# Performance work log

Hardware: AMD Instinct MI355X
Metric: run time of the kernel (lower is better)

The kernel has to match this reference:

```python
import jax, jax.numpy as jnp
import numpy as np

B, L, D = 4, 2048, 1024   # batch, seq_len, input_channels
S = 4096                  # param_token_num
DV = 1024                 # output_channels


def setup_inputs() -> dict:
    key = jax.random.key(0)
    k1, k2, k3 = jax.random.split(key, 3)
    return {
        "inputs": jax.random.normal(k1, (B, L, D), dtype=jnp.float32),
        "key_param_tokens": jax.random.normal(k2, (S, D), dtype=jnp.float32),
        "value_param_tokens": jax.random.normal(k3, (S, DV), dtype=jnp.float32),
    }


def reference(inputs, key_param_tokens, value_param_tokens):
    # scores: [B, L, S] — full score matrix (this is what a fused kernel would avoid)
    scores = jnp.einsum("bld,sd->bls", inputs, key_param_tokens)
    # gelu_l2_norm: exact (erf) gelu, then L2-normalize over S and rescale by sqrt(S)
    g = jax.nn.gelu(scores, approximate=False)
    l2 = jnp.linalg.norm(g, axis=-1, keepdims=True)
    w = g / l2 * jnp.sqrt(jnp.asarray(g.shape[-1], g.dtype))
    # weighted sum over param value tokens: [B, L, DV]
    return jnp.einsum("bls,sv->blv", w, value_param_tokens)
```

## Files before the change

kernel.cpp:

```cpp
#include <hip/hip_runtime.h>
#include <hip/hip_bf16.h>
#include <stdint.h>

#define M_ROWS 8192
#define D_DIM  1024
#define S_DIM  4096
#define DV_DIM 1024

typedef __attribute__((ext_vector_type(8))) short bf16x8;
typedef __attribute__((ext_vector_type(4))) float f32x4;
typedef unsigned short u16;

static __device__ __forceinline__ u16 f2bf(float x) {
  union { float f; unsigned u; } v; v.f = x;
  unsigned r = v.u + 0x7FFFu + ((v.u >> 16) & 1u);
  return (u16)(r >> 16);
}
static __device__ __forceinline__ float bf2f(u16 h) {
  union { unsigned u; float f; } v; v.u = ((unsigned)h) << 16;
  return v.f;
}
static __device__ __forceinline__ float gelu_fast(float x) {
  float u = 0.7978845608028654f * x * (1.0f + 0.044715f * x * x);
  float e = __expf(2.0f * u);
  float t = 1.0f - 2.0f / (e + 1.0f);
  return 0.5f * x * (1.0f + t);
}

static __device__ __forceinline__ void gload16(const void* g, void* l) {
  __builtin_amdgcn_global_load_lds(
      (__attribute__((address_space(1))) void*)(void*)(g),
      (__attribute__((address_space(3))) void*)(l), 16, 0, 0);
}

__global__ __launch_bounds__(256)
void cast_f32_bf16(const float* __restrict__ in, u16* __restrict__ out, int n4) {
  const int i = blockIdx.x * 256 + threadIdx.x;
  if (i >= n4) return;
  const float4 v = ((const float4*)in)[i];
  ushort4 o;
  o.x = f2bf(v.x); o.y = f2bf(v.y); o.z = f2bf(v.z); o.w = f2bf(v.w);
  ((ushort4*)out)[i] = o;
}

__global__ __launch_bounds__(256)
void transpose_cast(const float* __restrict__ V, u16* __restrict__ VT, int R, int C) {
  __shared__ float tile[32][33];
  const int tx = threadIdx.x & 31;
  const int ty = threadIdx.x >> 5;
  const int r0 = blockIdx.y * 32;
  const int c0 = blockIdx.x * 32;
#pragma unroll
  for (int dy = 0; dy < 32; dy += 8)
    tile[ty + dy][tx] = V[(long)(r0 + ty + dy) * C + (c0 + tx)];
  __syncthreads();
#pragma unroll
  for (int dy = 0; dy < 32; dy += 8)
    VT[(long)(c0 + ty + dy) * R + (r0 + tx)] = f2bf(tile[tx][ty + dy]);
}

__global__ __launch_bounds__(256)
void row_scale(const u16* __restrict__ G, float* __restrict__ scale, int S) {
  const int row = blockIdx.x;
  const u16* g = G + (long)row * S;
  float ssq = 0.f;
  for (int i = threadIdx.x * 8; i < S; i += 256 * 8) {
    bf16x8 v = *(const bf16x8*)&g[i];
#pragma unroll
    for (int j = 0; j < 8; ++j) {
      float f = bf2f((u16)v[j]);
      ssq += f * f;
    }
  }
#pragma unroll
  for (int off = 32; off > 0; off >>= 1)
    ssq += __shfl_down(ssq, off, 64);
  __shared__ float wsum[4];
  if ((threadIdx.x & 63) == 0) wsum[threadIdx.x >> 6] = ssq;
  __syncthreads();
  if (threadIdx.x == 0) {
    float t = wsum[0] + wsum[1] + wsum[2] + wsum[3];
    scale[row] = 64.0f * rsqrtf(t + 1e-30f);
  }
}


#define VM4 asm volatile("s_waitcnt vmcnt(4)" ::: "memory")
#define VM2 asm volatile("s_waitcnt vmcnt(2)" ::: "memory")
#define VM0 asm volatile("s_waitcnt vmcnt(0)" ::: "memory")

#define PHASE(P, STAGES, WAITS)                                               \
  {                                                                           \
    bf16x8 af[2][2];                                                          \
    _Pragma("unroll")                                                         \
    for (int j = 0; j < 2; ++j) {                                             \
      const int ar = wm * 128 + ((P) * 2 + j) * 16 + fr;                      \
      af[j][0] = rdfrag(la, ar, 0);                                           \
      af[j][1] = rdfrag(la, ar, 1);                                           \
    }                                                                         \
    STAGES;                                                                   \
    __builtin_amdgcn_s_barrier();                                             \
    asm volatile("s_waitcnt lgkmcnt(0)" ::: "memory");                        \
    __builtin_amdgcn_sched_barrier(0);                                        \
    __builtin_amdgcn_s_setprio(1);                                            \
    _Pragma("unroll")                                                         \
    for (int j = 0; j < 2; ++j) {                                             \
      _Pragma("unroll")                                                       \
      for (int n = 0; n < NF; ++n) {                                          \
        acc[(P) * 2 + j][n] = __builtin_amdgcn_mfma_f32_16x16x32_bf16(        \
            af[j][0], bfr[n][0], acc[(P) * 2 + j][n], 0, 0, 0);               \
        acc[(P) * 2 + j][n] = __builtin_amdgcn_mfma_f32_16x16x32_bf16(        \
            af[j][1], bfr[n][1], acc[(P) * 2 + j][n], 0, 0, 0);               \
      }                                                                       \
    }                                                                         \
    __builtin_amdgcn_s_setprio(0);                                            \
    WAITS;                                                                    \
    __builtin_amdgcn_s_barrier();                                             \
  }

#define READ_B                                                                \
  {                                                                           \
    _Pragma("unroll")                                                         \
    for (int n = 0; n < NF; ++n) {                                            \
      const int br = wn * WNT + n * 16 + fr;                                  \
      bfr[n][0] = rdfrag(lb, br, 0);                                          \
      bfr[n][1] = rdfrag(lb, br, 1);                                          \
    }                                                                         \
  }

template <int MODE, int BN>
__global__ __launch_bounds__(512, 2)
void gemm8p(const u16* __restrict__ A, const u16* __restrict__ Bm,
            void* __restrict__ Cout, const float* __restrict__ scale,
            const int K, const int N, const int nBN, const int nWG) {
  constexpr int BM = 256, BK = 64;
  constexpr int WNT = BN / 4;
  constexpr int NF = WNT / 16;

  __shared__ u16 ldsA[2][BM * BK];
  __shared__ u16 ldsB[2][BN * BK];

  const int tid = threadIdx.x;
  const int lane = tid & 63;
  const int wv = tid >> 6;
  const int wm = wv >> 2, wn = wv & 3;
  const int fr = lane & 15, hi = lane >> 4;

  int wg;
  {
    const int q = nWG >> 3, r = nWG & 7;
    const int x = blockIdx.x & 7, ix = blockIdx.x >> 3;
    wg = (x < r ? x * (q + 1) : r * (q + 1) + (x - r) * q) + ix;
  }
  const int bm = wg / nBN, bn = wg % nBN;
  const long aR0 = (long)bm * BM;
  const long bR0 = (long)bn * BN;

  const int srow = tid >> 3;
  const int sch = (tid & 7) ^ (srow & 7);
  const long aoff = (aR0 + srow) * (long)K + sch * 8;
  const long boff = (bR0 + srow) * (long)K + sch * 8;

  auto SA = [&](int buf, int r, int kOff) {
    gload16(A + aoff + ((long)r * 64) * K + kOff, &ldsA[buf][r * 4096 + tid * 8]);
  };
  auto SB = [&](int buf, int r, int kOff) {
    gload16(Bm + boff + ((long)r * 64) * K + kOff, &ldsB[buf][r * 4096 + tid * 8]);
  };
  auto rdfrag = [&](const u16* base, int row, int kk) -> bf16x8 {
    return *(const bf16x8*)&base[row * 64 + (((kk << 2) | hi) ^ (row & 7)) * 8];
  };

  f32x4 acc[8][NF];
#pragma unroll
  for (int m = 0; m < 8; ++m)
#pragma unroll
    for (int n = 0; n < NF; ++n)
      acc[m][n] = f32x4{0.f, 0.f, 0.f, 0.f};

  bf16x8 bfr[NF][2];
  const int nK = K / BK;

  if constexpr (BN == 256) {
    SB(0, 0, 0); SB(0, 1, 0); SB(0, 2, 0); SB(0, 3, 0);
  } else {
    SB(0, 0, 0); SB(0, 1, 0);
  }
  SA(0, 0, 0); SA(0, 2, 0); SA(0, 1, 0); SA(0, 3, 0);
  VM2;
  __builtin_amdgcn_s_barrier();

  int cur = 0;
  for (int kt = 0; kt < nK - 1; ++kt) {
    const int kN = (kt + 1) * BK;
    const int nxt = cur ^ 1;
    const u16* la = ldsA[cur];
    const u16* lb = ldsB[cur];
    READ_B;
    if constexpr (BN == 256) {
      PHASE(0, { SB(nxt, 0, kN); SB(nxt, 1, kN); }, {});
      PHASE(1, { SB(nxt, 2, kN); SB(nxt, 3, kN); }, VM4);
      PHASE(2, { SA(nxt, 0, kN); SA(nxt, 2, kN); }, {});
      PHASE(3, { SA(nxt, 1, kN); SA(nxt, 3, kN); }, VM2);
    } else {
      PHASE(0, { SB(nxt, 0, kN); SB(nxt, 1, kN); }, {});
      PHASE(1, { SA(nxt, 0, kN); SA(nxt, 2, kN); }, VM4);
      PHASE(2, { SA(nxt, 1, kN); SA(nxt, 3, kN); }, {});
      PHASE(3, {}, VM2);
    }
    cur ^= 1;
  }

  {
    const u16* la = ldsA[cur];
    const u16* lb = ldsB[cur];
    READ_B;
    PHASE(0, {}, {});
    PHASE(1, {}, VM0);
    PHASE(2, {}, {});
    PHASE(3, {}, {});
  }

  const long row0 = aR0 + wm * 128;
  const long col0 = bR0 + wn * WNT;
  if constexpr (MODE == 0) {
    u16* Cg = (u16*)Cout;
#pragma unroll
    for (int m = 0; m < 8; ++m) {
#pragma unroll
      for (int i = 0; i < 4; ++i) {
        const long r = row0 + m * 16 + hi * 4 + i;
#pragma unroll
        for (int n = 0; n < NF; ++n)
          Cg[r * N + col0 + n * 16 + fr] = f2bf(gelu_fast(acc[m][n][i]));
      }
    }
  } else {
    float* Cf = (float*)Cout;
#pragma unroll
    for (int m = 0; m < 8; ++m) {
#pragma unroll
      for (int i = 0; i < 4; ++i) {
        const long r = row0 + m * 16 + hi * 4 + i;
        const float s = scale[r];
#pragma unroll
        for (int n = 0; n < NF; ++n)
          Cf[r * N + col0 + n * 16 + fr] = acc[m][n][i] * s;
      }
    }
  }
}

extern "C" void kernel_launch(void* const* d_in, const int* in_sizes, int n_in,
                              void* d_out, int out_size, void* d_ws, size_t ws_size,
                              hipStream_t stream) {
  const float* Qf = (const float*)d_in[0];
  const float* Kf = (const float*)d_in[1];
  const float* Vf = (const float*)d_in[2];
  float* Out = (float*)d_out;

  const int M = M_ROWS, D = D_DIM, S = S_DIM, DV = DV_DIM;

  char* p = (char*)d_ws;
  u16* Qb = (u16*)p;            p += (size_t)M * D * 2;
  u16* Kb = (u16*)p;            p += (size_t)S * D * 2;
  u16* VT = (u16*)p;            p += (size_t)DV * S * 2;
  float* scalebuf = (float*)p;  p += (size_t)M * 4;
  u16* G = (u16*)p;
  const size_t fixed = (size_t)(p - (char*)d_ws);
  const size_t avail = (ws_size > fixed) ? (ws_size - fixed) : 0;

  const size_t bytes_per_row = (size_t)S * 2;
  size_t rows_fit = avail / bytes_per_row;
  int chunk = (int)((rows_fit / 256) * 256);
  if (chunk > M) chunk = M;
  if (chunk < 256) chunk = 256;

  cast_f32_bf16<<<(M * D / 4 + 255) / 256, 256, 0, stream>>>(Qf, Qb, M * D / 4);
  cast_f32_bf16<<<(S * D / 4 + 255) / 256, 256, 0, stream>>>(Kf, Kb, S * D / 4);
  transpose_cast<<<dim3(DV / 32, S / 32), 256, 0, stream>>>(Vf, VT, S, DV);

  const int nBN1 = S / 256;
  const int nBN2 = DV / 128;
  for (int m0 = 0; m0 < M; m0 += chunk) {
    const int rows = (M - m0 < chunk) ? (M - m0) : chunk;
    const int nWG1 = (rows / 256) * nBN1;
    gemm8p<0, 256><<<dim3(nWG1), 512, 0, stream>>>(
        Qb + (size_t)m0 * D, Kb, (void*)G, nullptr, D, S, nBN1, nWG1);
    row_scale<<<rows, 256, 0, stream>>>(G, scalebuf, S);
    const int nWG2 = (rows / 256) * nBN2;
    gemm8p<1, 128><<<dim3(nWG2), 512, 0, stream>>>(
        G, VT, (void*)(Out + (size_t)m0 * DV), scalebuf, S, DV, nBN2, nWG2);
  }
}
```

Baseline: 197.5 us.

## Fuse row sum-of-squares into first GEMM epilogue and restructure prefetch pipeline

The first GEMM epilogue now accumulates the squared GELU values per row and tile, reduces them across lanes and waves through LDS, and writes per-tile partial sums. A small finalize kernel then turns these into row scales. This replaces the row_scale pass that re-read the full bf16 score matrix. The first GEMM also switches to a 2x4 wave layout instead of 4x2, and the K loop prefetches B two tiles ahead and A one tile ahead with retuned vmcnt waits. The risks are a larger epilogue, an extra partial-sum buffer, and subtle wait-count correctness in the new pipeline.

```diff
diff --git a/kernel.cpp b/kernel.cpp
--- a/kernel.cpp
+++ b/kernel.cpp
@@ -60,61 +60,44 @@
 }
 
 __global__ __launch_bounds__(256)
-void row_scale(const u16* __restrict__ G, float* __restrict__ scale, int S) {
-  const int row = blockIdx.x;
-  const u16* g = G + (long)row * S;
-  float ssq = 0.f;
-  for (int i = threadIdx.x * 8; i < S; i += 256 * 8) {
-    bf16x8 v = *(const bf16x8*)&g[i];
-#pragma unroll
-    for (int j = 0; j < 8; ++j) {
-      float f = bf2f((u16)v[j]);
-      ssq += f * f;
-    }
-  }
-#pragma unroll
-  for (int off = 32; off > 0; off >>= 1)
-    ssq += __shfl_down(ssq, off, 64);
-  __shared__ float wsum[4];
-  if ((threadIdx.x & 63) == 0) wsum[threadIdx.x >> 6] = ssq;
-  __syncthreads();
-  if (threadIdx.x == 0) {
-    float t = wsum[0] + wsum[1] + wsum[2] + wsum[3];
-    scale[row] = 64.0f * rsqrtf(t + 1e-30f);
-  }
-}
-
-
-#define VM4 asm volatile("s_waitcnt vmcnt(4)" ::: "memory")
-#define VM2 asm volatile("s_waitcnt vmcnt(2)" ::: "memory")
-#define VM0 asm volatile("s_waitcnt vmcnt(0)" ::: "memory")
-
-#define PHASE(P, STAGES, WAITS)                                               \
+void finalize_scale(const float* __restrict__ Pp, float* __restrict__ scale,
+                    int nBN, int rows) {
+  const int r = blockIdx.x * 256 + threadIdx.x;
+  if (r >= rows) return;
+  float s = 0.f;
+  for (int j = 0; j < nBN; ++j) s += Pp[(long)r * nBN + j];
+  scale[r] = 64.0f * rsqrtf(s + 1e-30f);
+}
+
+
+#define VMW(N) asm volatile("s_waitcnt vmcnt(" #N ")" ::: "memory")
+
+#define PH(P, STG, WT)                                                        \
   {                                                                           \
-    bf16x8 af[2][2];                                                          \
+    bf16x8 af[MF][2];                                                         \
     _Pragma("unroll")                                                         \
-    for (int j = 0; j < 2; ++j) {                                             \
-      const int ar = wm * 128 + ((P) * 2 + j) * 16 + fr;                      \
+    for (int j = 0; j < MF; ++j) {                                            \
+      const int ar = wm * MSPAN + ((P) * MF + j) * 16 + fr;                   \
       af[j][0] = rdfrag(la, ar, 0);                                           \
       af[j][1] = rdfrag(la, ar, 1);                                           \
     }                                                                         \
-    STAGES;                                                                   \
+    STG;                                                                      \
     __builtin_amdgcn_s_barrier();                                             \
     asm volatile("s_waitcnt lgkmcnt(0)" ::: "memory");                        \
     __builtin_amdgcn_sched_barrier(0);                                        \
     __builtin_amdgcn_s_setprio(1);                                            \
     _Pragma("unroll")                                                         \
-    for (int j = 0; j < 2; ++j) {                                             \
+    for (int j = 0; j < MF; ++j) {                                            \
       _Pragma("unroll")                                                       \
       for (int n = 0; n < NF; ++n) {                                          \
-        acc[(P) * 2 + j][n] = __builtin_amdgcn_mfma_f32_16x16x32_bf16(        \
-            af[j][0], bfr[n][0], acc[(P) * 2 + j][n], 0, 0, 0);               \
-        acc[(P) * 2 + j][n] = __builtin_amdgcn_mfma_f32_16x16x32_bf16(        \
-            af[j][1], bfr[n][1], acc[(P) * 2 + j][n], 0, 0, 0);               \
+        acc[(P) * MF + j][n] = __builtin_amdgcn_mfma_f32_16x16x32_bf16(       \
+            af[j][0], bfr[n][0], acc[(P) * MF + j][n], 0, 0, 0);              \
+        acc[(P) * MF + j][n] = __builtin_amdgcn_mfma_f32_16x16x32_bf16(       \
+            af[j][1], bfr[n][1], acc[(P) * MF + j][n], 0, 0, 0);              \
       }                                                                       \
     }                                                                         \
     __builtin_amdgcn_s_setprio(0);                                            \
-    WAITS;                                                                    \
+    WT;                                                                       \
     __builtin_amdgcn_s_barrier();                                             \
   }
 
@@ -122,20 +105,46 @@
   {                                                                           \
     _Pragma("unroll")                                                         \
     for (int n = 0; n < NF; ++n) {                                            \
-      const int br = wn * WNT + n * 16 + fr;                                  \
+      const int br = wn * NSPAN + n * 16 + fr;                                \
       bfr[n][0] = rdfrag(lb, br, 0);                                          \
       bfr[n][1] = rdfrag(lb, br, 1);                                          \
     }                                                                         \
   }
 
-template <int MODE, int BN>
+#define TILE(SAEN, SBEN, W1, W3)                                              \
+  {                                                                           \
+    const u16* la = ldsA[kt & 1];                                             \
+    const u16* lb = ldsB[kt & 1];                                             \
+    const int bA = (kt + 1) & 1;                                              \
+    const int bB = kt & 1;                                                    \
+    const long kA = (long)(kt + 1) * BK;                                      \
+    const long kB = (long)(kt + 2) * BK;                                      \
+    READ_B;                                                                   \
+    if constexpr (BN == 256) {                                                \
+      PH(0, if (SAEN) { SA(bA, 0, kA); SA(bA, 2, kA); }, {});                 \
+      PH(1, if (SAEN) { SA(bA, 1, kA); SA(bA, 3, kA); }, W1);                 \
+      PH(2, if (SBEN) { SB(bB, 0, kB); SB(bB, 1, kB); }, {});                 \
+      PH(3, if (SBEN) { SB(bB, 2, kB); SB(bB, 3, kB); }, W3);                 \
+    } else {                                                                  \
+      PH(0, if (SAEN) { SA(bA, 0, kA); SA(bA, 1, kA); }, {});                 \
+      PH(1, if (SAEN) { SA(bA, 2, kA); SA(bA, 3, kA); }, {});                 \
+      PH(2, if (SBEN) { SB(bB, 0, kB); SB(bB, 1, kB); }, {});                 \
+      PH(3, {}, W3);                                                          \
+    }                                                                         \
+  }
+
+template <int MODE, int BN, int WM>
 __global__ __launch_bounds__(512, 2)
 void gemm8p(const u16* __restrict__ A, const u16* __restrict__ Bm,
-            void* __restrict__ Cout, const float* __restrict__ scale,
+            void* __restrict__ Cout, float* __restrict__ Pp,
+            const float* __restrict__ scale,
             const int K, const int N, const int nBN, const int nWG) {
   constexpr int BM = 256, BK = 64;
-  constexpr int WNT = BN / 4;
-  constexpr int NF = WNT / 16;
+  constexpr int WN = 8 / WM;
+  constexpr int MSPAN = BM / WM;
+  constexpr int NSPAN = BN / WN;
+  constexpr int MF = MSPAN / 64;
+  constexpr int NF = NSPAN / 16;
 
   __shared__ u16 ldsA[2][BM * BK];
   __shared__ u16 ldsB[2][BN * BK];
@@ -143,7 +152,7 @@
   const int tid = threadIdx.x;
   const int lane = tid & 63;
   const int wv = tid >> 6;
-  const int wm = wv >> 2, wn = wv & 3;
+  const int wm = wv / WN, wn = wv % WN;
   const int fr = lane & 15, hi = lane >> 4;
 
   int wg;
@@ -161,19 +170,19 @@
   const long aoff = (aR0 + srow) * (long)K + sch * 8;
   const long boff = (bR0 + srow) * (long)K + sch * 8;
 
-  auto SA = [&](int buf, int r, int kOff) {
-    gload16(A + aoff + ((long)r * 64) * K + kOff, &ldsA[buf][r * 4096 + tid * 8]);
+  auto SA = [&](int buf, int r, long kOff) {
+    gload16(A + aoff + (long)r * 64 * K + kOff, &ldsA[buf][r * 4096 + tid * 8]);
   };
-  auto SB = [&](int buf, int r, int kOff) {
-    gload16(Bm + boff + ((long)r * 64) * K + kOff, &ldsB[buf][r * 4096 + tid * 8]);
+  auto SB = [&](int buf, int r, long kOff) {
+    gload16(Bm + boff + (long)r * 64 * K + kOff, &ldsB[buf][r * 4096 + tid * 8]);
   };
   auto rdfrag = [&](const u16* base, int row, int kk) -> bf16x8 {
     return *(const bf16x8*)&base[row * 64 + (((kk << 2) | hi) ^ (row & 7)) * 8];
   };
 
-  f32x4 acc[8][NF];
-#pragma unroll
-  for (int m = 0; m < 8; ++m)
+  f32x4 acc[4 * MF][NF];
+#pragma unroll
+  for (int m = 0; m < 4 * MF; ++m)
 #pragma unroll
     for (int n = 0; n < NF; ++n)
       acc[m][n] = f32x4{0.f, 0.f, 0.f, 0.f};
@@ -183,69 +192,67 @@
 
   if constexpr (BN == 256) {
     SB(0, 0, 0); SB(0, 1, 0); SB(0, 2, 0); SB(0, 3, 0);
+    SA(0, 0, 0); SA(0, 2, 0); SA(0, 1, 0); SA(0, 3, 0);
+    SB(1, 0, BK); SB(1, 1, BK); SB(1, 2, BK); SB(1, 3, BK);
+    VMW(6);
   } else {
     SB(0, 0, 0); SB(0, 1, 0);
-  }
-  SA(0, 0, 0); SA(0, 2, 0); SA(0, 1, 0); SA(0, 3, 0);
-  VM2;
+    SA(0, 0, 0); SA(0, 1, 0); SA(0, 2, 0); SA(0, 3, 0);
+    SB(1, 0, BK); SB(1, 1, BK);
+    VMW(2);
+  }
   __builtin_amdgcn_s_barrier();
 
-  int cur = 0;
-  for (int kt = 0; kt < nK - 1; ++kt) {
-    const int kN = (kt + 1) * BK;
-    const int nxt = cur ^ 1;
-    const u16* la = ldsA[cur];
-    const u16* lb = ldsB[cur];
-    READ_B;
-    if constexpr (BN == 256) {
-      PHASE(0, { SB(nxt, 0, kN); SB(nxt, 1, kN); }, {});
-      PHASE(1, { SB(nxt, 2, kN); SB(nxt, 3, kN); }, VM4);
-      PHASE(2, { SA(nxt, 0, kN); SA(nxt, 2, kN); }, {});
-      PHASE(3, { SA(nxt, 1, kN); SA(nxt, 3, kN); }, VM2);
-    } else {
-      PHASE(0, { SB(nxt, 0, kN); SB(nxt, 1, kN); }, {});
-      PHASE(1, { SA(nxt, 0, kN); SA(nxt, 2, kN); }, VM4);
-      PHASE(2, { SA(nxt, 1, kN); SA(nxt, 3, kN); }, {});
-      PHASE(3, {}, VM2);
-    }
-    cur ^= 1;
-  }
-
-  {
-    const u16* la = ldsA[cur];
-    const u16* lb = ldsB[cur];
-    READ_B;
-    PHASE(0, {}, {});
-    PHASE(1, {}, VM0);
-    PHASE(2, {}, {});
-    PHASE(3, {}, {});
-  }
-
-  const long row0 = aR0 + wm * 128;
-  const long col0 = bR0 + wn * WNT;
+  int kt = 0;
+  if constexpr (BN == 256) {
+    for (; kt < nK - 2; ++kt) TILE(true, true, VMW(8), VMW(6));
+    TILE(true, false, VMW(8), VMW(2)); ++kt;
+    TILE(false, false, VMW(0), {});
+  } else {
+    for (; kt < nK - 2; ++kt) TILE(true, true, {}, VMW(2));
+    TILE(true, false, {}, VMW(0)); ++kt;
+    TILE(false, false, {}, {});
+  }
+
   if constexpr (MODE == 0) {
     u16* Cg = (u16*)Cout;
-#pragma unroll
-    for (int m = 0; m < 8; ++m) {
+    float* red = (float*)&ldsA[0][0];
+#pragma unroll
+    for (int m = 0; m < 4 * MF; ++m) {
 #pragma unroll
       for (int i = 0; i < 4; ++i) {
-        const long r = row0 + m * 16 + hi * 4 + i;
-#pragma unroll
-        for (int n = 0; n < NF; ++n)
-          Cg[r * N + col0 + n * 16 + fr] = f2bf(gelu_fast(acc[m][n][i]));
+        const int rl = wm * MSPAN + m * 16 + hi * 4 + i;
+        const long r = aR0 + rl;
+        float s = 0.f;
+#pragma unroll
+        for (int n = 0; n < NF; ++n) {
+          const float g = gelu_fast(acc[m][n][i]);
+          Cg[r * N + bR0 + wn * NSPAN + n * 16 + fr] = f2bf(g);
+          s += g * g;
+        }
+        s += __shfl_xor(s, 1); s += __shfl_xor(s, 2);
+        s += __shfl_xor(s, 4); s += __shfl_xor(s, 8);
+        if (fr == 0) red[rl * WN + wn] = s;
       }
+    }
+    __syncthreads();
+    if (tid < BM) {
+      float s = 0.f;
+#pragma unroll
+      for (int w = 0; w < WN; ++w) s += red[tid * WN + w];
+      Pp[(aR0 + tid) * nBN + bn] = s;
     }
   } else {
     float* Cf = (float*)Cout;
 #pragma unroll
-    for (int m = 0; m < 8; ++m) {
+    for (int m = 0; m < 4 * MF; ++m) {
 #pragma unroll
       for (int i = 0; i < 4; ++i) {
-        const long r = row0 + m * 16 + hi * 4 + i;
+        const long r = aR0 + wm * MSPAN + m * 16 + hi * 4 + i;
         const float s = scale[r];
 #pragma unroll
         for (int n = 0; n < NF; ++n)
-          Cf[r * N + col0 + n * 16 + fr] = acc[m][n][i] * s;
+          Cf[r * N + bR0 + wn * NSPAN + n * 16 + fr] = acc[m][n][i] * s;
       }
     }
   }
@@ -260,12 +267,15 @@
   float* Out = (float*)d_out;
 
   const int M = M_ROWS, D = D_DIM, S = S_DIM, DV = DV_DIM;
+  const int nBN1 = S / 256;
+  const int nBN2 = DV / 128;
 
   char* p = (char*)d_ws;
   u16* Qb = (u16*)p;            p += (size_t)M * D * 2;
   u16* Kb = (u16*)p;            p += (size_t)S * D * 2;
   u16* VT = (u16*)p;            p += (size_t)DV * S * 2;
   float* scalebuf = (float*)p;  p += (size_t)M * 4;
+  float* Pp = (float*)p;        p += (size_t)M * nBN1 * 4;
   u16* G = (u16*)p;
   const size_t fixed = (size_t)(p - (char*)d_ws);
   const size_t avail = (ws_size > fixed) ? (ws_size - fixed) : 0;
@@ -280,16 +290,14 @@
   cast_f32_bf16<<<(S * D / 4 + 255) / 256, 256, 0, stream>>>(Kf, Kb, S * D / 4);
   transpose_cast<<<dim3(DV / 32, S / 32), 256, 0, stream>>>(Vf, VT, S, DV);
 
-  const int nBN1 = S / 256;
-  const int nBN2 = DV / 128;
   for (int m0 = 0; m0 < M; m0 += chunk) {
     const int rows = (M - m0 < chunk) ? (M - m0) : chunk;
     const int nWG1 = (rows / 256) * nBN1;
-    gemm8p<0, 256><<<dim3(nWG1), 512, 0, stream>>>(
-        Qb + (size_t)m0 * D, Kb, (void*)G, nullptr, D, S, nBN1, nWG1);
-    row_scale<<<rows, 256, 0, stream>>>(G, scalebuf, S);
+    gemm8p<0, 256, 2><<<dim3(nWG1), 512, 0, stream>>>(
+        Qb + (size_t)m0 * D, Kb, (void*)G, Pp, nullptr, D, S, nBN1, nWG1);
+    finalize_scale<<<(rows + 255) / 256, 256, 0, stream>>>(Pp, scalebuf, nBN1, rows);
     const int nWG2 = (rows / 256) * nBN2;
-    gemm8p<1, 128><<<dim3(nWG2), 512, 0, stream>>>(
-        G, VT, (void*)(Out + (size_t)m0 * DV), scalebuf, S, DV, nBN2, nWG2);
-  }
-}
+    gemm8p<1, 128, 4><<<dim3(nWG2), 512, 0, stream>>>(
+        G, VT, (void*)(Out + (size_t)m0 * DV), nullptr, scalebuf, S, DV, nBN2, nWG2);
+  }
+}
```

After: 215.9 us. 9.3% more time.

## Split-K second GEMM into two halves with 256-wide tiles plus reduction kernel

Applied to the files above, without the earlier changes.

The second GEMM (scaled G times V) is now split along K into two halves. Each half runs on separate workgroups with 256x256 tiles instead of 256x128, and the halves write to Out and a scratch buffer P1. An elementwise add kernel then sums the two partials. This keeps the same number of workgroups while using larger tiles for better operand reuse, at the cost of an extra fp32 partial write and read plus one more launch. The split path is taken only when the whole problem fits in one chunk and the workspace can hold the extra partial buffer.

```diff
diff --git a/kernel.cpp b/kernel.cpp
--- a/kernel.cpp
+++ b/kernel.cpp
@@ -81,6 +81,16 @@
   if (threadIdx.x == 0) {
     float t = wsum[0] + wsum[1] + wsum[2] + wsum[3];
     scale[row] = 64.0f * rsqrtf(t + 1e-30f);
+  }
+}
+
+__global__ __launch_bounds__(256)
+void add_inplace(float* __restrict__ Out, const float* __restrict__ P1, int n4) {
+  for (int i = blockIdx.x * 256 + threadIdx.x; i < n4; i += 2048 * 256) {
+    float4 a = ((const float4*)Out)[i];
+    const float4 b = ((const float4*)P1)[i];
+    a.x += b.x; a.y += b.y; a.z += b.z; a.w += b.w;
+    ((float4*)Out)[i] = a;
   }
 }
 
@@ -128,11 +138,13 @@
     }                                                                         \
   }
 
-template <int MODE, int BN>
+template <int MODE, int BN, bool SPLITK>
 __global__ __launch_bounds__(512, 2)
 void gemm8p(const u16* __restrict__ A, const u16* __restrict__ Bm,
-            void* __restrict__ Cout, const float* __restrict__ scale,
-            const int K, const int N, const int nBN, const int nWG) {
+            void* __restrict__ Cout0, void* __restrict__ Cout1,
+            const float* __restrict__ scale,
+            const int K, const int lda, const int ldb,
+            const int N, const int nBN, const int nWG) {
   constexpr int BM = 256, BK = 64;
   constexpr int WNT = BN / 4;
   constexpr int NF = WNT / 16;
@@ -152,20 +164,29 @@
     const int x = blockIdx.x & 7, ix = blockIdx.x >> 3;
     wg = (x < r ? x * (q + 1) : r * (q + 1) + (x - r) * q) + ix;
   }
+  void* Cout = Cout0;
+  if constexpr (SPLITK) {
+    const int half = nWG >> 1;
+    const int ks = (wg >= half) ? 1 : 0;
+    wg -= ks * half;
+    A += (long)ks * K;
+    Bm += (long)ks * K;
+    if (ks) Cout = Cout1;
+  }
   const int bm = wg / nBN, bn = wg % nBN;
   const long aR0 = (long)bm * BM;
   const long bR0 = (long)bn * BN;
 
   const int srow = tid >> 3;
   const int sch = (tid & 7) ^ (srow & 7);
-  const long aoff = (aR0 + srow) * (long)K + sch * 8;
-  const long boff = (bR0 + srow) * (long)K + sch * 8;
+  const long aoff = (aR0 + srow) * (long)lda + sch * 8;
+  const long boff = (bR0 + srow) * (long)ldb + sch * 8;
 
   auto SA = [&](int buf, int r, int kOff) {
-    gload16(A + aoff + ((long)r * 64) * K + kOff, &ldsA[buf][r * 4096 + tid * 8]);
+    gload16(A + aoff + ((long)r * 64) * lda + kOff, &ldsA[buf][r * 4096 + tid * 8]);
   };
   auto SB = [&](int buf, int r, int kOff) {
-    gload16(Bm + boff + ((long)r * 64) * K + kOff, &ldsB[buf][r * 4096 + tid * 8]);
+    gload16(Bm + boff + ((long)r * 64) * ldb + kOff, &ldsB[buf][r * 4096 + tid * 8]);
   };
   auto rdfrag = [&](const u16* base, int row, int kk) -> bf16x8 {
     return *(const bf16x8*)&base[row * 64 + (((kk << 2) | hi) ^ (row & 7)) * 8];
@@ -276,6 +297,11 @@
   if (chunk > M) chunk = M;
   if (chunk < 256) chunk = 256;
 
+  const size_t Gbytes = (size_t)M * S * 2;
+  const size_t Pbytes = (size_t)M * DV * 4;
+  const bool use_split = (chunk >= M) && (avail >= Gbytes + Pbytes);
+  float* P1 = (float*)((char*)G + Gbytes);
+
   cast_f32_bf16<<<(M * D / 4 + 255) / 256, 256, 0, stream>>>(Qf, Qb, M * D / 4);
   cast_f32_bf16<<<(S * D / 4 + 255) / 256, 256, 0, stream>>>(Kf, Kb, S * D / 4);
   transpose_cast<<<dim3(DV / 32, S / 32), 256, 0, stream>>>(Vf, VT, S, DV);
@@ -285,11 +311,19 @@
   for (int m0 = 0; m0 < M; m0 += chunk) {
     const int rows = (M - m0 < chunk) ? (M - m0) : chunk;
     const int nWG1 = (rows / 256) * nBN1;
-    gemm8p<0, 256><<<dim3(nWG1), 512, 0, stream>>>(
-        Qb + (size_t)m0 * D, Kb, (void*)G, nullptr, D, S, nBN1, nWG1);
+    gemm8p<0, 256, false><<<dim3(nWG1), 512, 0, stream>>>(
+        Qb + (size_t)m0 * D, Kb, (void*)G, nullptr, nullptr, D, D, D, S, nBN1, nWG1);
     row_scale<<<rows, 256, 0, stream>>>(G, scalebuf, S);
-    const int nWG2 = (rows / 256) * nBN2;
-    gemm8p<1, 128><<<dim3(nWG2), 512, 0, stream>>>(
-        G, VT, (void*)(Out + (size_t)m0 * DV), scalebuf, S, DV, nBN2, nWG2);
-  }
-}
+    if (use_split) {
+      const int nBNs = DV / 256;
+      const int nWGs = 2 * (M / 256) * nBNs;
+      gemm8p<1, 256, true><<<dim3(nWGs), 512, 0, stream>>>(
+          G, VT, (void*)Out, (void*)P1, scalebuf, S / 2, S, S, DV, nBNs, nWGs);
+      add_inplace<<<2048, 256, 0, stream>>>(Out, P1, M * DV / 4);
+    } else {
+      const int nWG2 = (rows / 256) * nBN2;
+      gemm8p<1, 128, false><<<dim3(nWG2), 512, 0, stream>>>(
+          G, VT, (void*)(Out + (size_t)m0 * DV), nullptr, scalebuf, S, S, S, DV, nBN2, nWG2);
+    }
+  }
+}
```

Result: faster. 192.5 us (-2.6%).

## Replace 256x256 8-wave GEMM tiles with 128x128 4-wave tiles

Applied to the files above, without the earlier changes.

Both GEMMs now use a single kernel with 128x128 output tiles and 256 threads (4 waves, each covering a 64x64 subtile) in place of the 8-wave 256-wide tiles. Each block loads half as many rows per stage, and the launch grid grows fourfold for the first GEMM and twofold for the second. The intent is to raise occupancy and block count for better load balance across CUs. The cost is lower arithmetic intensity per tile, so more global and LDS traffic per flop.

```diff
diff --git a/kernel.cpp b/kernel.cpp
--- a/kernel.cpp
+++ b/kernel.cpp
@@ -91,27 +91,20 @@
 
 #define PHASE(P, STAGES, WAITS)                                               \
   {                                                                           \
-    bf16x8 af[2][2];                                                          \
-    _Pragma("unroll")                                                         \
-    for (int j = 0; j < 2; ++j) {                                             \
-      const int ar = wm * 128 + ((P) * 2 + j) * 16 + fr;                      \
-      af[j][0] = rdfrag(la, ar, 0);                                           \
-      af[j][1] = rdfrag(la, ar, 1);                                           \
-    }                                                                         \
+    const int ar = wm * 64 + (P) * 16 + fr;                                   \
+    bf16x8 af0 = rdfrag(la, ar, 0);                                           \
+    bf16x8 af1 = rdfrag(la, ar, 1);                                           \
     STAGES;                                                                   \
     __builtin_amdgcn_s_barrier();                                             \
     asm volatile("s_waitcnt lgkmcnt(0)" ::: "memory");                        \
     __builtin_amdgcn_sched_barrier(0);                                        \
     __builtin_amdgcn_s_setprio(1);                                            \
     _Pragma("unroll")                                                         \
-    for (int j = 0; j < 2; ++j) {                                             \
-      _Pragma("unroll")                                                       \
-      for (int n = 0; n < NF; ++n) {                                          \
-        acc[(P) * 2 + j][n] = __builtin_amdgcn_mfma_f32_16x16x32_bf16(        \
-            af[j][0], bfr[n][0], acc[(P) * 2 + j][n], 0, 0, 0);               \
-        acc[(P) * 2 + j][n] = __builtin_amdgcn_mfma_f32_16x16x32_bf16(        \
-            af[j][1], bfr[n][1], acc[(P) * 2 + j][n], 0, 0, 0);               \
-      }                                                                       \
+    for (int n = 0; n < 4; ++n) {                                             \
+      acc[(P)][n] = __builtin_amdgcn_mfma_f32_16x16x32_bf16(                  \
+          af0, bfr[n][0], acc[(P)][n], 0, 0, 0);                              \
+      acc[(P)][n] = __builtin_amdgcn_mfma_f32_16x16x32_bf16(                  \
+          af1, bfr[n][1], acc[(P)][n], 0, 0, 0);                              \
     }                                                                         \
     __builtin_amdgcn_s_setprio(0);                                            \
     WAITS;                                                                    \
@@ -121,21 +114,19 @@
 #define READ_B                                                                \
   {                                                                           \
     _Pragma("unroll")                                                         \
-    for (int n = 0; n < NF; ++n) {                                            \
-      const int br = wn * WNT + n * 16 + fr;                                  \
+    for (int n = 0; n < 4; ++n) {                                             \
+      const int br = wn * 64 + n * 16 + fr;                                   \
       bfr[n][0] = rdfrag(lb, br, 0);                                          \
       bfr[n][1] = rdfrag(lb, br, 1);                                          \
     }                                                                         \
   }
 
-template <int MODE, int BN>
-__global__ __launch_bounds__(512, 2)
-void gemm8p(const u16* __restrict__ A, const u16* __restrict__ Bm,
+template <int MODE>
+__global__ __launch_bounds__(256, 2)
+void gemm4w(const u16* __restrict__ A, const u16* __restrict__ Bm,
             void* __restrict__ Cout, const float* __restrict__ scale,
             const int K, const int N, const int nBN, const int nWG) {
-  constexpr int BM = 256, BK = 64;
-  constexpr int WNT = BN / 4;
-  constexpr int NF = WNT / 16;
+  constexpr int BM = 128, BN = 128, BK = 64;
 
   __shared__ u16 ldsA[2][BM * BK];
   __shared__ u16 ldsB[2][BN * BK];
@@ -143,7 +134,7 @@
   const int tid = threadIdx.x;
   const int lane = tid & 63;
   const int wv = tid >> 6;
-  const int wm = wv >> 2, wn = wv & 3;
+  const int wm = wv >> 1, wn = wv & 1;
   const int fr = lane & 15, hi = lane >> 4;
 
   int wg;
@@ -162,30 +153,26 @@
   const long boff = (bR0 + srow) * (long)K + sch * 8;
 
   auto SA = [&](int buf, int r, int kOff) {
-    gload16(A + aoff + ((long)r * 64) * K + kOff, &ldsA[buf][r * 4096 + tid * 8]);
+    gload16(A + aoff + ((long)r * 32) * K + kOff, &ldsA[buf][r * 2048 + tid * 8]);
   };
   auto SB = [&](int buf, int r, int kOff) {
-    gload16(Bm + boff + ((long)r * 64) * K + kOff, &ldsB[buf][r * 4096 + tid * 8]);
+    gload16(Bm + boff + ((long)r * 32) * K + kOff, &ldsB[buf][r * 2048 + tid * 8]);
   };
   auto rdfrag = [&](const u16* base, int row, int kk) -> bf16x8 {
     return *(const bf16x8*)&base[row * 64 + (((kk << 2) | hi) ^ (row & 7)) * 8];
   };
 
-  f32x4 acc[8][NF];
-#pragma unroll
-  for (int m = 0; m < 8; ++m)
-#pragma unroll
-    for (int n = 0; n < NF; ++n)
+  f32x4 acc[4][4];
+#pragma unroll
+  for (int m = 0; m < 4; ++m)
+#pragma unroll
+    for (int n = 0; n < 4; ++n)
       acc[m][n] = f32x4{0.f, 0.f, 0.f, 0.f};
 
-  bf16x8 bfr[NF][2];
+  bf16x8 bfr[4][2];
   const int nK = K / BK;
 
-  if constexpr (BN == 256) {
-    SB(0, 0, 0); SB(0, 1, 0); SB(0, 2, 0); SB(0, 3, 0);
-  } else {
-    SB(0, 0, 0); SB(0, 1, 0);
-  }
+  SB(0, 0, 0); SB(0, 1, 0); SB(0, 2, 0); SB(0, 3, 0);
   SA(0, 0, 0); SA(0, 2, 0); SA(0, 1, 0); SA(0, 3, 0);
   VM2;
   __builtin_amdgcn_s_barrier();
@@ -197,17 +184,10 @@
     const u16* la = ldsA[cur];
     const u16* lb = ldsB[cur];
     READ_B;
-    if constexpr (BN == 256) {
-      PHASE(0, { SB(nxt, 0, kN); SB(nxt, 1, kN); }, {});
-      PHASE(1, { SB(nxt, 2, kN); SB(nxt, 3, kN); }, VM4);
-      PHASE(2, { SA(nxt, 0, kN); SA(nxt, 2, kN); }, {});
-      PHASE(3, { SA(nxt, 1, kN); SA(nxt, 3, kN); }, VM2);
-    } else {
-      PHASE(0, { SB(nxt, 0, kN); SB(nxt, 1, kN); }, {});
-      PHASE(1, { SA(nxt, 0, kN); SA(nxt, 2, kN); }, VM4);
-      PHASE(2, { SA(nxt, 1, kN); SA(nxt, 3, kN); }, {});
-      PHASE(3, {}, VM2);
-    }
+    PHASE(0, { SB(nxt, 0, kN); SB(nxt, 1, kN); }, {});
+    PHASE(1, { SB(nxt, 2, kN); SB(nxt, 3, kN); }, VM4);
+    PHASE(2, { SA(nxt, 0, kN); SA(nxt, 2, kN); }, {});
+    PHASE(3, { SA(nxt, 1, kN); SA(nxt, 3, kN); }, VM2);
     cur ^= 1;
   }
 
@@ -221,30 +201,30 @@
     PHASE(3, {}, {});
   }
 
-  const long row0 = aR0 + wm * 128;
-  const long col0 = bR0 + wn * WNT;
+  const long row0 = aR0 + wm * 64;
+  const long col0 = bR0 + wn * 64;
   if constexpr (MODE == 0) {
     u16* Cg = (u16*)Cout;
 #pragma unroll
-    for (int m = 0; m < 8; ++m) {
+    for (int m = 0; m < 4; ++m) {
 #pragma unroll
       for (int i = 0; i < 4; ++i) {
         const long r = row0 + m * 16 + hi * 4 + i;
 #pragma unroll
-        for (int n = 0; n < NF; ++n)
+        for (int n = 0; n < 4; ++n)
           Cg[r * N + col0 + n * 16 + fr] = f2bf(gelu_fast(acc[m][n][i]));
       }
     }
   } else {
     float* Cf = (float*)Cout;
 #pragma unroll
-    for (int m = 0; m < 8; ++m) {
+    for (int m = 0; m < 4; ++m) {
 #pragma unroll
       for (int i = 0; i < 4; ++i) {
         const long r = row0 + m * 16 + hi * 4 + i;
         const float s = scale[r];
 #pragma unroll
-        for (int n = 0; n < NF; ++n)
+        for (int n = 0; n < 4; ++n)
           Cf[r * N + col0 + n * 16 + fr] = acc[m][n][i] * s;
       }
     }
@@ -272,24 +252,24 @@
 
   const size_t bytes_per_row = (size_t)S * 2;
   size_t rows_fit = avail / bytes_per_row;
-  int chunk = (int)((rows_fit / 256) * 256);
+  int chunk = (int)((rows_fit / 128) * 128);
   if (chunk > M) chunk = M;
-  if (chunk < 256) chunk = 256;
+  if (chunk < 128) chunk = 128;
 
   cast_f32_bf16<<<(M * D / 4 + 255) / 256, 256, 0, stream>>>(Qf, Qb, M * D / 4);
   cast_f32_bf16<<<(S * D / 4 + 255) / 256, 256, 0, stream>>>(Kf, Kb, S * D / 4);
   transpose_cast<<<dim3(DV / 32, S / 32), 256, 0, stream>>>(Vf, VT, S, DV);
 
-  const int nBN1 = S / 256;
+  const int nBN1 = S / 128;
   const int nBN2 = DV / 128;
   for (int m0 = 0; m0 < M; m0 += chunk) {
     const int rows = (M - m0 < chunk) ? (M - m0) : chunk;
-    const int nWG1 = (rows / 256) * nBN1;
-    gemm8p<0, 256><<<dim3(nWG1), 512, 0, stream>>>(
+    const int nWG1 = (rows / 128) * nBN1;
+    gemm4w<0><<<dim3(nWG1), 256, 0, stream>>>(
         Qb + (size_t)m0 * D, Kb, (void*)G, nullptr, D, S, nBN1, nWG1);
     row_scale<<<rows, 256, 0, stream>>>(G, scalebuf, S);
-    const int nWG2 = (rows / 256) * nBN2;
-    gemm8p<1, 128><<<dim3(nWG2), 512, 0, stream>>>(
+    const int nWG2 = (rows / 128) * nBN2;
+    gemm4w<1><<<dim3(nWG2), 256, 0, stream>>>(
         G, VT, (void*)(Out + (size_t)m0 * DV), scalebuf, S, DV, nBN2, nWG2);
   }
 }
```

After: 203.6 us. +3.1%, slower.
